# Performance work log

Measured on AMD Instinct MI355X. Metric: run time of the kernel, lower is better.

The kernel has to match this reference:

```python
import jax, jax.numpy as jnp
import numpy as np

N = 100000
E = 1600000
D = 128
H = 128


def gcn_conv(x, W, b, src, dst, n_nodes):
    # x: [N, Din] -> linear transform first (PyG GCNConv)
    h = x @ W  # [N, Dout]
    # add self loops
    loop = jnp.arange(n_nodes, dtype=src.dtype)
    s = jnp.concatenate([src, loop])
    d = jnp.concatenate([dst, loop])
    # symmetric normalization: deg computed on destination (col) with unit weights
    deg = jnp.zeros((n_nodes,), dtype=h.dtype).at[d].add(1.0)
    dinv = jnp.where(deg > 0, jax.lax.rsqrt(deg), 0.0)
    norm = dinv[s] * dinv[d]  # [E+N]
    msg = h[s] * norm[:, None]  # gather + scale
    out = jax.ops.segment_sum(msg, d, num_segments=n_nodes)
    return out + b


def setup_inputs() -> dict:
    key = jax.random.key(0)
    ks = jax.random.split(key, 8)
    x = jax.random.normal(ks[0], (N, D), dtype=jnp.float32)
    edge_index = jax.random.randint(ks[1], (2, E), 0, N, dtype=jnp.int32)
    sc = 1.0 / np.sqrt(D)
    gate_W = jax.random.uniform(ks[2], (D, D), jnp.float32, -sc, sc)
    gate_b = jax.random.uniform(ks[3], (D,), jnp.float32, -sc, sc)
    W1 = jax.random.normal(ks[4], (D, H), dtype=jnp.float32) * sc
    b1 = jnp.zeros((H,), jnp.float32)
    W2 = jax.random.normal(ks[5], (H, H), dtype=jnp.float32) * (1.0 / np.sqrt(H))
    b2 = jnp.zeros((H,), jnp.float32)
    return {"x": x, "edge_index": edge_index, "gate_W": gate_W, "gate_b": gate_b,
            "W1": W1, "b1": b1, "W2": W2, "b2": b2}


def reference(x, edge_index, gate_W, gate_b, W1, b1, W2, b2):
    src, dst = edge_index[0], edge_index[1]
    gate = jax.nn.sigmoid(x @ gate_W + gate_b)
    h = x * gate
    h = gcn_conv(h, W1, b1, src, dst, N)
    h = jax.nn.relu(h)
    h = gcn_conv(h, W2, b2, src, dst, N)
    return h
```

## Files before the change

### kernel.cpp

```cpp
#include <hip/hip_runtime.h>
#include <hip/hip_bf16.h>
#include <math.h>


#define BUCKET_SHIFT 8
#define BUCKET_W 256
#define CAP 4864
#define NB_MAX 512
#define OSTRIDE 136

typedef __attribute__((ext_vector_type(8))) short bf16x8;
typedef __attribute__((ext_vector_type(4))) float f32x4;

__device__ __forceinline__ unsigned short f2bf(float x) {
    unsigned int u = __float_as_uint(x);
    unsigned int r = (u + 0x7FFFu + ((u >> 16) & 1u)) >> 16;
    return (unsigned short)r;
}
__device__ __forceinline__ float blo(unsigned int u) { return __uint_as_float(u << 16); }
__device__ __forceinline__ float bhi(unsigned int u) { return __uint_as_float(u & 0xFFFF0000u); }

__device__ __forceinline__ void cvt_hilo8(const float* v, bf16x8& hi, bf16x8& lo) {
#pragma unroll
    for (int j = 0; j < 8; j++) {
        unsigned short h = f2bf(v[j]);
        float hf = __uint_as_float((unsigned int)h << 16);
        hi[j] = (short)h;
        lo[j] = (short)f2bf(v[j] - hf);
    }
}

__device__ __forceinline__ f32x4 MF(bf16x8 a, bf16x8 b, f32x4 c) {
    return __builtin_amdgcn_mfma_f32_16x16x32_bf16(a, b, c, 0, 0, 0);
}

__global__ __launch_bounds__(512)
void prepinit_kernel(const float* __restrict__ W0, const float* __restrict__ W1,
                     const float* __restrict__ W2, uint4* __restrict__ img,
                     int* __restrict__ bcursor, int NB) {
    int b = blockIdx.x, t = threadIdx.x;
    if (b < 12) {
        int idx = b * 512 + t;
        int c = idx & 127, kb = (idx >> 7) & 15, w = idx >> 11;
        const float* W = (w == 0) ? W0 : (w == 1) ? W1 : W2;
        bf16x8 hb;
#pragma unroll
        for (int j = 0; j < 8; j++) hb[j] = (short)f2bf(W[(size_t)(kb * 8 + j) * 128 + c]);
        img[w * 2048 + c * 16 + (kb ^ (c & 15))] = *(uint4*)&hb;
    } else {
        if (t < NB) bcursor[t] = 0;
    }
}

__device__ __forceinline__ void partition_body(char* smem, int b, int t,
                                               const int* __restrict__ src,
                                               const int* __restrict__ dst,
                                               int* __restrict__ bucketCursor,
                                               unsigned int* __restrict__ part,
                                               int E, int NB, int chunk) {
    int* hist  = (int*)smem;
    int* basec = hist + NB_MAX;
    int e0 = b * chunk;
    int e1 = min(E, e0 + chunk);

    for (int i = t; i < NB; i += 512) hist[i] = 0;
    __syncthreads();
    for (int e = e0 + t; e < e1; e += 512) {
        int bb = dst[e] >> BUCKET_SHIFT;
        atomicAdd(&hist[bb], 1);
    }
    __syncthreads();
    for (int i = t; i < NB; i += 512) {
        int c = hist[i];
        basec[i] = c ? atomicAdd(&bucketCursor[i], c) : 0;
    }
    __syncthreads();
    for (int i = t; i < NB; i += 512) hist[i] = 0;
    __syncthreads();
    for (int e = e0 + t; e < e1; e += 512) {
        int d = dst[e], s = src[e];
        int bb = d >> BUCKET_SHIFT;
        int r = atomicAdd(&hist[bb], 1);
        int pos = basec[bb] + r;
        if (pos < CAP)
            part[(size_t)bb * CAP + pos] = ((unsigned int)(d & (BUCKET_W - 1)) << 17) | (unsigned int)s;
    }
}

__device__ __forceinline__ void gate_body(char* smem, int gb, int t,
                                          const float* __restrict__ x,
                                          const uint4* __restrict__ gimg,
                                          const float* __restrict__ gate_b,
                                          unsigned short* __restrict__ hpack, int n) {
    uint4* Wl = (uint4*)smem;
    unsigned short* OutS = (unsigned short*)(smem + 32768);
    int lane = t & 63, wv = t >> 6;
    int blockRow = gb * 128;

    for (int idx = t; idx < 2048; idx += 512) Wl[idx] = gimg[idx];

    bf16x8 Ahi[4], Alo[4];
    {
        int arow = blockRow + wv * 16 + (lane & 15);
        const float* ap = x + (size_t)min(arow, n - 1) * 128 + (lane >> 4) * 8;
#pragma unroll
        for (int s = 0; s < 4; s++) {
            float v[8];
            *(float4*)&v[0] = *(const float4*)&ap[s * 32];
            *(float4*)&v[4] = *(const float4*)&ap[s * 32 + 4];
            cvt_hilo8(v, Ahi[s], Alo[s]);
        }
    }
    __syncthreads();

    f32x4 acc[8];
#pragma unroll
    for (int nt = 0; nt < 8; nt++) acc[nt] = (f32x4)(0.f);
#pragma unroll
    for (int s = 0; s < 4; s++) {
        int kb = s * 4 + (lane >> 4);
#pragma unroll
        for (int nt = 0; nt < 8; nt++) {
            int c = nt * 16 + (lane & 15);
            bf16x8 bh = *(bf16x8*)&Wl[c * 16 + (kb ^ (lane & 15))];
            acc[nt] = MF(Ahi[s], bh, acc[nt]);
            acc[nt] = MF(Alo[s], bh, acc[nt]);
        }
    }

    int rl0 = wv * 16 + (lane >> 4) * 4;
#pragma unroll
    for (int nt = 0; nt < 8; nt++) {
        int c = nt * 16 + (lane & 15);
        float gb2 = gate_b[c];
#pragma unroll
        for (int r = 0; r < 4; r++) {
            int grow = min(blockRow + rl0 + r, n - 1);
            float xv = x[(size_t)grow * 128 + c];
            float hv = xv / (1.f + __expf(-(acc[nt][r] + gb2)));
            OutS[(rl0 + r) * OSTRIDE + c] = f2bf(hv);
        }
    }
    __syncthreads();
    {
        int row = t >> 2;
        int c0 = (t & 3) * 32;
        int grow = blockRow + row;
        if (grow < n) {
#pragma unroll
            for (int j = 0; j < 4; j++) {
                uint4 v = *(uint4*)&OutS[row * OSTRIDE + c0 + j * 8];
                *(uint4*)&hpack[(size_t)grow * 128 + c0 + j * 8] = v;
            }
        }
    }
}

__global__ __launch_bounds__(512)
void pg_kernel(const int* __restrict__ src, const int* __restrict__ dst,
               int* __restrict__ bucketCursor, unsigned int* __restrict__ part,
               int E, int NB, int chunk,
               const float* __restrict__ x, const uint4* __restrict__ gimg,
               const float* __restrict__ gate_b, unsigned short* __restrict__ hpack, int n) {
    __shared__ __align__(16) char smem[67584];
    int b = blockIdx.x, t = threadIdx.x;
    if (b < 256) partition_body(smem, b, t, src, dst, bucketCursor, part, E, NB, chunk);
    else         gate_body(smem, b - 256, t, x, gimg, gate_b, hpack, n);
}

__global__ __launch_bounds__(512)
void bucket_scan_kernel(const int* __restrict__ bucketCursor,
                        int* __restrict__ bucketBase, int NB) {
    __shared__ int sm[NB_MAX];
    int t = threadIdx.x;
    int v = (t < NB) ? min(bucketCursor[t], CAP) : 0;
    sm[t] = v;
    __syncthreads();
    for (int off = 1; off < NB_MAX; off <<= 1) {
        int a = (t >= off) ? sm[t - off] : 0;
        __syncthreads();
        sm[t] += a;
        __syncthreads();
    }
    if (t < NB) bucketBase[t + 1] = sm[t];
    if (t == 0) bucketBase[0] = 0;
}

__device__ __forceinline__ void fill_body(char* smem, int b, int t,
                                          const unsigned int* __restrict__ part,
                                          const int* __restrict__ bucketBase,
                                          int* __restrict__ rowptr, float* __restrict__ dinv,
                                          int* __restrict__ col, int N, int NB) {
    unsigned int* eLDS = (unsigned int*)smem;
    int* deg  = (int*)(smem + CAP * 4);
    int* cur  = deg + BUCKET_W;
    int* wsum = cur + BUCKET_W;

    int base = bucketBase[b];
    int cnt = bucketBase[b + 1] - base;

    for (int i = t; i < cnt; i += 512) eLDS[i] = part[(size_t)b * CAP + i];
    if (t < 256) deg[t] = 0;
    __syncthreads();
    for (int i = t; i < cnt; i += 512) atomicAdd(&deg[eLDS[i] >> 17], 1);
    __syncthreads();

    int v = (t < 256) ? deg[t] : 0;
    int incl = v;
    int lane = t & 63, w = t >> 6;
    for (int off = 1; off < 64; off <<= 1) {
        int u = __shfl_up(incl, off, 64);
        if (lane >= off) incl += u;
    }
    if (lane == 63) wsum[w] = incl;
    __syncthreads();
    int add = 0;
#pragma unroll
    for (int j = 0; j < 4; j++) if (j < w) add += wsum[j];
    int excl = add + incl - v;
    if (t < 256) {
        cur[t] = excl;
        int gnode = b * BUCKET_W + t;
        if (gnode < N) {
            rowptr[gnode] = base + excl;
            dinv[gnode] = rsqrtf((float)(v + 1));
        }
    }
    if (b == NB - 1 && t == 0) rowptr[N] = base + cnt;
    __syncthreads();

    for (int i = t; i < cnt; i += 512) {
        unsigned int ev = eLDS[i];
        int dl = ev >> 17;
        int p = atomicAdd(&cur[dl], 1);
        col[base + p] = (int)(ev & 0x1FFFFu);
    }
}

__device__ __forceinline__ void gemm_body(char* smem, int gb, int t,
                                          const unsigned short* __restrict__ A,
                                          const uint4* __restrict__ wimg,
                                          unsigned short* __restrict__ g, int n) {
    uint4* Wl = (uint4*)smem;
    unsigned short* OutS = (unsigned short*)(smem + 32768);
    int lane = t & 63, wv = t >> 6;
    int blockRow = gb * 128;

    for (int idx = t; idx < 2048; idx += 512) Wl[idx] = wimg[idx];

    bf16x8 Af[4];
    {
        int arow = blockRow + wv * 16 + (lane & 15);
        const uint4* ap = (const uint4*)(A + (size_t)min(arow, n - 1) * 128);
#pragma unroll
        for (int s = 0; s < 4; s++) {
            uint4 u = ap[(lane >> 4) + s * 4];
            Af[s] = *(bf16x8*)&u;
        }
    }
    __syncthreads();

    f32x4 acc[8];
#pragma unroll
    for (int nt = 0; nt < 8; nt++) acc[nt] = (f32x4)(0.f);
#pragma unroll
    for (int s = 0; s < 4; s++) {
        int kb = s * 4 + (lane >> 4);
#pragma unroll
        for (int nt = 0; nt < 8; nt++) {
            int c = nt * 16 + (lane & 15);
            bf16x8 bh = *(bf16x8*)&Wl[c * 16 + (kb ^ (lane & 15))];
            acc[nt] = MF(Af[s], bh, acc[nt]);
        }
    }

    int rl0 = wv * 16 + (lane >> 4) * 4;
#pragma unroll
    for (int nt = 0; nt < 8; nt++) {
        int c = nt * 16 + (lane & 15);
#pragma unroll
        for (int r = 0; r < 4; r++)
            OutS[(rl0 + r) * OSTRIDE + c] = f2bf(acc[nt][r]);
    }
    __syncthreads();
    {
        int row = t >> 2;
        int c0 = (t & 3) * 32;
        int grow = blockRow + row;
        if (grow < n) {
#pragma unroll
            for (int j = 0; j < 4; j++) {
                uint4 v = *(uint4*)&OutS[row * OSTRIDE + c0 + j * 8];
                *(uint4*)&g[(size_t)grow * 128 + c0 + j * 8] = v;
            }
        }
    }
}

__global__ __launch_bounds__(512)
void fg_kernel(const unsigned int* __restrict__ part, const int* __restrict__ bucketBase,
               int* __restrict__ rowptr, float* __restrict__ dinv, int* __restrict__ col,
               int N, int NB,
               const unsigned short* __restrict__ A, const uint4* __restrict__ wimg,
               unsigned short* __restrict__ g) {
    __shared__ __align__(16) char smem[67584];
    int b = blockIdx.x, t = threadIdx.x;
    if (b < NB) fill_body(smem, b, t, part, bucketBase, rowptr, dinv, col, N, NB);
    else        gemm_body(smem, b - NB, t, A, wimg, g, N);
}

__global__ __launch_bounds__(256)
void spmm_gemm_kernel(const uint4* __restrict__ g16, const int* __restrict__ rowptr,
                      const int* __restrict__ col, const float* __restrict__ dinv,
                      const float* __restrict__ b1, const uint4* __restrict__ w2img,
                      unsigned short* __restrict__ g2, int n) {
    __shared__ __align__(16) char smem[16896];
    uint4* Hl = (uint4*)smem;
    unsigned short* OutS = (unsigned short*)(smem + 8192);

    int t = threadIdx.x;
    int blockRow = blockIdx.x * 32;

    int r = t >> 3, l = t & 7;
    int i = min(blockRow + r, n - 1);
    float di = dinv[i];

    float acc[16];
    {
        uint4 s0 = g16[(size_t)i * 16 + l];
        uint4 s1 = g16[(size_t)i * 16 + 8 + l];
        acc[0] = di * blo(s0.x);  acc[1] = di * bhi(s0.x);
        acc[2] = di * blo(s0.y);  acc[3] = di * bhi(s0.y);
        acc[4] = di * blo(s0.z);  acc[5] = di * bhi(s0.z);
        acc[6] = di * blo(s0.w);  acc[7] = di * bhi(s0.w);
        acc[8] = di * blo(s1.x);  acc[9] = di * bhi(s1.x);
        acc[10] = di * blo(s1.y); acc[11] = di * bhi(s1.y);
        acc[12] = di * blo(s1.z); acc[13] = di * bhi(s1.z);
        acc[14] = di * blo(s1.w); acc[15] = di * bhi(s1.w);
    }
    int e0 = rowptr[i], e1 = rowptr[i + 1];
    int e = e0;
    for (; e + 4 <= e1; e += 4) {
        int s0 = col[e], s1 = col[e + 1], s2 = col[e + 2], s3 = col[e + 3];
        uint4 a0 = g16[(size_t)s0 * 16 + l];
        uint4 a1 = g16[(size_t)s0 * 16 + 8 + l];
        uint4 c0 = g16[(size_t)s1 * 16 + l];
        uint4 c1 = g16[(size_t)s1 * 16 + 8 + l];
        uint4 d0 = g16[(size_t)s2 * 16 + l];
        uint4 d1 = g16[(size_t)s2 * 16 + 8 + l];
        uint4 f0 = g16[(size_t)s3 * 16 + l];
        uint4 f1 = g16[(size_t)s3 * 16 + 8 + l];
        float w0 = dinv[s0], w1 = dinv[s1], w2 = dinv[s2], w3 = dinv[s3];
        acc[0]  = fmaf(w0, blo(a0.x), fmaf(w1, blo(c0.x), fmaf(w2, blo(d0.x), fmaf(w3, blo(f0.x), acc[0]))));
        acc[1]  = fmaf(w0, bhi(a0.x), fmaf(w1, bhi(c0.x), fmaf(w2, bhi(d0.x), fmaf(w3, bhi(f0.x), acc[1]))));
        acc[2]  = fmaf(w0, blo(a0.y), fmaf(w1, blo(c0.y), fmaf(w2, blo(d0.y), fmaf(w3, blo(f0.y), acc[2]))));
        acc[3]  = fmaf(w0, bhi(a0.y), fmaf(w1, bhi(c0.y), fmaf(w2, bhi(d0.y), fmaf(w3, bhi(f0.y), acc[3]))));
        acc[4]  = fmaf(w0, blo(a0.z), fmaf(w1, blo(c0.z), fmaf(w2, blo(d0.z), fmaf(w3, blo(f0.z), acc[4]))));
        acc[5]  = fmaf(w0, bhi(a0.z), fmaf(w1, bhi(c0.z), fmaf(w2, bhi(d0.z), fmaf(w3, bhi(f0.z), acc[5]))));
        acc[6]  = fmaf(w0, blo(a0.w), fmaf(w1, blo(c0.w), fmaf(w2, blo(d0.w), fmaf(w3, blo(f0.w), acc[6]))));
        acc[7]  = fmaf(w0, bhi(a0.w), fmaf(w1, bhi(c0.w), fmaf(w2, bhi(d0.w), fmaf(w3, bhi(f0.w), acc[7]))));
        acc[8]  = fmaf(w0, blo(a1.x), fmaf(w1, blo(c1.x), fmaf(w2, blo(d1.x), fmaf(w3, blo(f1.x), acc[8]))));
        acc[9]  = fmaf(w0, bhi(a1.x), fmaf(w1, bhi(c1.x), fmaf(w2, bhi(d1.x), fmaf(w3, bhi(f1.x), acc[9]))));
        acc[10] = fmaf(w0, blo(a1.y), fmaf(w1, blo(c1.y), fmaf(w2, blo(d1.y), fmaf(w3, blo(f1.y), acc[10]))));
        acc[11] = fmaf(w0, bhi(a1.y), fmaf(w1, bhi(c1.y), fmaf(w2, bhi(d1.y), fmaf(w3, bhi(f1.y), acc[11]))));
        acc[12] = fmaf(w0, blo(a1.z), fmaf(w1, blo(c1.z), fmaf(w2, blo(d1.z), fmaf(w3, blo(f1.z), acc[12]))));
        acc[13] = fmaf(w0, bhi(a1.z), fmaf(w1, bhi(c1.z), fmaf(w2, bhi(d1.z), fmaf(w3, bhi(f1.z), acc[13]))));
        acc[14] = fmaf(w0, blo(a1.w), fmaf(w1, blo(c1.w), fmaf(w2, blo(d1.w), fmaf(w3, blo(f1.w), acc[14]))));
        acc[15] = fmaf(w0, bhi(a1.w), fmaf(w1, bhi(c1.w), fmaf(w2, bhi(d1.w), fmaf(w3, bhi(f1.w), acc[15]))));
    }
    for (; e < e1; e++) {
        int s0 = col[e];
        uint4 a0 = g16[(size_t)s0 * 16 + l];
        uint4 a1 = g16[(size_t)s0 * 16 + 8 + l];
        float w0 = dinv[s0];
        acc[0]  = fmaf(w0, blo(a0.x), acc[0]);  acc[1]  = fmaf(w0, bhi(a0.x), acc[1]);
        acc[2]  = fmaf(w0, blo(a0.y), acc[2]);  acc[3]  = fmaf(w0, bhi(a0.y), acc[3]);
        acc[4]  = fmaf(w0, blo(a0.z), acc[4]);  acc[5]  = fmaf(w0, bhi(a0.z), acc[5]);
        acc[6]  = fmaf(w0, blo(a0.w), acc[6]);  acc[7]  = fmaf(w0, bhi(a0.w), acc[7]);
        acc[8]  = fmaf(w0, blo(a1.x), acc[8]);  acc[9]  = fmaf(w0, bhi(a1.x), acc[9]);
        acc[10] = fmaf(w0, blo(a1.y), acc[10]); acc[11] = fmaf(w0, bhi(a1.y), acc[11]);
        acc[12] = fmaf(w0, blo(a1.z), acc[12]); acc[13] = fmaf(w0, bhi(a1.z), acc[13]);
        acc[14] = fmaf(w0, blo(a1.w), acc[14]); acc[15] = fmaf(w0, bhi(a1.w), acc[15]);
    }

    {
        const float* bp0 = b1 + l * 8;
        const float* bp1 = b1 + 64 + l * 8;
        float4 b00 = *(const float4*)&bp0[0], b01 = *(const float4*)&bp0[4];
        float4 b10 = *(const float4*)&bp1[0], b11 = *(const float4*)&bp1[4];
        float h[16];
        h[0] = fmaxf(fmaf(acc[0], di, b00.x), 0.f);
        h[1] = fmaxf(fmaf(acc[1], di, b00.y), 0.f);
        h[2] = fmaxf(fmaf(acc[2], di, b00.z), 0.f);
        h[3] = fmaxf(fmaf(acc[3], di, b00.w), 0.f);
        h[4] = fmaxf(fmaf(acc[4], di, b01.x), 0.f);
        h[5] = fmaxf(fmaf(acc[5], di, b01.y), 0.f);
        h[6] = fmaxf(fmaf(acc[6], di, b01.z), 0.f);
        h[7] = fmaxf(fmaf(acc[7], di, b01.w), 0.f);
        h[8] = fmaxf(fmaf(acc[8], di, b10.x), 0.f);
        h[9] = fmaxf(fmaf(acc[9], di, b10.y), 0.f);
        h[10] = fmaxf(fmaf(acc[10], di, b10.z), 0.f);
        h[11] = fmaxf(fmaf(acc[11], di, b10.w), 0.f);
        h[12] = fmaxf(fmaf(acc[12], di, b11.x), 0.f);
        h[13] = fmaxf(fmaf(acc[13], di, b11.y), 0.f);
        h[14] = fmaxf(fmaf(acc[14], di, b11.z), 0.f);
        h[15] = fmaxf(fmaf(acc[15], di, b11.w), 0.f);
        uint4 p0, p1;
        p0.x = (unsigned int)f2bf(h[0]) | ((unsigned int)f2bf(h[1]) << 16);
        p0.y = (unsigned int)f2bf(h[2]) | ((unsigned int)f2bf(h[3]) << 16);
        p0.z = (unsigned int)f2bf(h[4]) | ((unsigned int)f2bf(h[5]) << 16);
        p0.w = (unsigned int)f2bf(h[6]) | ((unsigned int)f2bf(h[7]) << 16);
        p1.x = (unsigned int)f2bf(h[8]) | ((unsigned int)f2bf(h[9]) << 16);
        p1.y = (unsigned int)f2bf(h[10]) | ((unsigned int)f2bf(h[11]) << 16);
        p1.z = (unsigned int)f2bf(h[12]) | ((unsigned int)f2bf(h[13]) << 16);
        p1.w = (unsigned int)f2bf(h[14]) | ((unsigned int)f2bf(h[15]) << 16);
        int sw = r & 15;
        Hl[r * 16 + (l ^ sw)] = p0;
        Hl[r * 16 + ((l + 8) ^ sw)] = p1;
    }
    __syncthreads();

    int lane = t & 63, wv = t >> 6;
    int rt = wv & 1, ch = wv >> 1;
    bf16x8 Af[4];
    {
        int arow = rt * 16 + (lane & 15);
        int asw = arow & 15;
#pragma unroll
        for (int s = 0; s < 4; s++) {
            int kb = s * 4 + (lane >> 4);
            uint4 u = Hl[arow * 16 + (kb ^ asw)];
            Af[s] = *(bf16x8*)&u;
        }
    }
    f32x4 acc2[4];
#pragma unroll
    for (int ntl = 0; ntl < 4; ntl++) acc2[ntl] = (f32x4)(0.f);
#pragma unroll
    for (int s = 0; s < 4; s++) {
        int kb = s * 4 + (lane >> 4);
#pragma unroll
        for (int ntl = 0; ntl < 4; ntl++) {
            int c = (ch * 4 + ntl) * 16 + (lane & 15);
            uint4 u = w2img[c * 16 + (kb ^ (lane & 15))];
            acc2[ntl] = MF(Af[s], *(bf16x8*)&u, acc2[ntl]);
        }
    }

    int rl0 = rt * 16 + (lane >> 4) * 4;
    float dr[4];
#pragma unroll
    for (int rr = 0; rr < 4; rr++) dr[rr] = dinv[min(blockRow + rl0 + rr, n - 1)];
#pragma unroll
    for (int ntl = 0; ntl < 4; ntl++) {
        int c = (ch * 4 + ntl) * 16 + (lane & 15);
#pragma unroll
        for (int rr = 0; rr < 4; rr++)
            OutS[(rl0 + rr) * OSTRIDE + c] = f2bf(acc2[ntl][rr] * dr[rr]);
    }
    __syncthreads();
    {
        int grow = blockRow + r;
        if (grow < n) {
            uint4 v0 = *(uint4*)&OutS[r * OSTRIDE + l * 16];
            uint4 v1 = *(uint4*)&OutS[r * OSTRIDE + l * 16 + 8];
            *(uint4*)&g2[(size_t)grow * 128 + l * 16] = v0;
            *(uint4*)&g2[(size_t)grow * 128 + l * 16 + 8] = v1;
        }
    }
}

__global__ void spmm_kernel(const uint4* __restrict__ g16, const int* __restrict__ rowptr,
                            const int* __restrict__ col, const float* __restrict__ dinv,
                            const float* __restrict__ bias, float* __restrict__ outv,
                            int n, int nhb) {
    int half = (blockIdx.x >= nhb) ? 1 : 0;
    int rb = blockIdx.x - half * nhb;
    int i = rb * 32 + (threadIdx.x >> 3);
    if (i >= n) return;
    int c = threadIdx.x & 7;

    const uint4* gp = g16 + half * 8 + c;
    float acc[8];
    uint4 sv = gp[(size_t)i * 16];
    acc[0] = blo(sv.x); acc[1] = bhi(sv.x);
    acc[2] = blo(sv.y); acc[3] = bhi(sv.y);
    acc[4] = blo(sv.z); acc[5] = bhi(sv.z);
    acc[6] = blo(sv.w); acc[7] = bhi(sv.w);

    int e0 = rowptr[i], e1 = rowptr[i + 1];
    int e = e0;
    for (; e + 8 <= e1; e += 8) {
        uint4 v0 = gp[(size_t)col[e] * 16];
        uint4 v1 = gp[(size_t)col[e + 1] * 16];
        uint4 v2 = gp[(size_t)col[e + 2] * 16];
        uint4 v3 = gp[(size_t)col[e + 3] * 16];
        uint4 v4 = gp[(size_t)col[e + 4] * 16];
        uint4 v5 = gp[(size_t)col[e + 5] * 16];
        uint4 v6 = gp[(size_t)col[e + 6] * 16];
        uint4 v7 = gp[(size_t)col[e + 7] * 16];
        acc[0] += ((blo(v0.x) + blo(v1.x)) + (blo(v2.x) + blo(v3.x))) +
                  ((blo(v4.x) + blo(v5.x)) + (blo(v6.x) + blo(v7.x)));
        acc[1] += ((bhi(v0.x) + bhi(v1.x)) + (bhi(v2.x) + bhi(v3.x))) +
                  ((bhi(v4.x) + bhi(v5.x)) + (bhi(v6.x) + bhi(v7.x)));
        acc[2] += ((blo(v0.y) + blo(v1.y)) + (blo(v2.y) + blo(v3.y))) +
                  ((blo(v4.y) + blo(v5.y)) + (blo(v6.y) + blo(v7.y)));
        acc[3] += ((bhi(v0.y) + bhi(v1.y)) + (bhi(v2.y) + bhi(v3.y))) +
                  ((bhi(v4.y) + bhi(v5.y)) + (bhi(v6.y) + bhi(v7.y)));
        acc[4] += ((blo(v0.z) + blo(v1.z)) + (blo(v2.z) + blo(v3.z))) +
                  ((blo(v4.z) + blo(v5.z)) + (blo(v6.z) + blo(v7.z)));
        acc[5] += ((bhi(v0.z) + bhi(v1.z)) + (bhi(v2.z) + bhi(v3.z))) +
                  ((bhi(v4.z) + bhi(v5.z)) + (bhi(v6.z) + bhi(v7.z)));
        acc[6] += ((blo(v0.w) + blo(v1.w)) + (blo(v2.w) + blo(v3.w))) +
                  ((blo(v4.w) + blo(v5.w)) + (blo(v6.w) + blo(v7.w)));
        acc[7] += ((bhi(v0.w) + bhi(v1.w)) + (bhi(v2.w) + bhi(v3.w))) +
                  ((bhi(v4.w) + bhi(v5.w)) + (bhi(v6.w) + bhi(v7.w)));
    }
    for (; e + 2 <= e1; e += 2) {
        uint4 v0 = gp[(size_t)col[e] * 16];
        uint4 v1 = gp[(size_t)col[e + 1] * 16];
        acc[0] += blo(v0.x) + blo(v1.x); acc[1] += bhi(v0.x) + bhi(v1.x);
        acc[2] += blo(v0.y) + blo(v1.y); acc[3] += bhi(v0.y) + bhi(v1.y);
        acc[4] += blo(v0.z) + blo(v1.z); acc[5] += bhi(v0.z) + bhi(v1.z);
        acc[6] += blo(v0.w) + blo(v1.w); acc[7] += bhi(v0.w) + bhi(v1.w);
    }
    if (e < e1) {
        uint4 v0 = gp[(size_t)col[e] * 16];
        acc[0] += blo(v0.x); acc[1] += bhi(v0.x);
        acc[2] += blo(v0.y); acc[3] += bhi(v0.y);
        acc[4] += blo(v0.z); acc[5] += bhi(v0.z);
        acc[6] += blo(v0.w); acc[7] += bhi(v0.w);
    }

    float di = dinv[i];
    const float4* b4 = (const float4*)(bias + half * 64);
    float4 bv0 = b4[c * 2], bv1 = b4[c * 2 + 1];
    float r0[8];
    r0[0] = fmaf(acc[0], di, bv0.x);
    r0[1] = fmaf(acc[1], di, bv0.y);
    r0[2] = fmaf(acc[2], di, bv0.z);
    r0[3] = fmaf(acc[3], di, bv0.w);
    r0[4] = fmaf(acc[4], di, bv1.x);
    r0[5] = fmaf(acc[5], di, bv1.y);
    r0[6] = fmaf(acc[6], di, bv1.z);
    r0[7] = fmaf(acc[7], di, bv1.w);
    float* o = outv + (size_t)i * 128 + half * 64 + c * 8;
    f32x4 a = *(f32x4*)&r0[0];
    f32x4 b = *(f32x4*)&r0[4];
    __builtin_nontemporal_store(a, (f32x4*)o);
    __builtin_nontemporal_store(b, (f32x4*)(o + 4));
}

extern "C" void kernel_launch(void* const* d_in, const int* in_sizes, int n_in,
                              void* d_out, int out_size, void* d_ws, size_t ws_size,
                              hipStream_t stream) {
    const float* x      = (const float*)d_in[0];
    const int*   ei     = (const int*)d_in[1];
    const float* gate_W = (const float*)d_in[2];
    const float* gate_b = (const float*)d_in[3];
    const float* W1     = (const float*)d_in[4];
    const float* b1     = (const float*)d_in[5];
    const float* W2     = (const float*)d_in[6];
    const float* b2     = (const float*)d_in[7];
    float* out = (float*)d_out;

    const int N = in_sizes[0] / 128;
    const int E = in_sizes[1] / 2;
    const int* src = ei;
    const int* dst = ei + E;
    const int NB = (N + BUCKET_W - 1) / BUCKET_W;

    char* p = (char*)d_ws;
    auto alloc = [&](size_t bytes) { char* q = p; p += (bytes + 255) & ~(size_t)255; return q; };
    int*   rowptr  = (int*)alloc(((size_t)N + 1) * 4);
    float* dinv    = (float*)alloc((size_t)N * 4);
    int*   colb    = (int*)alloc((size_t)E * 4);
    int*   bcursor = (int*)alloc((size_t)NB * 4);
    int*   bbase   = (int*)alloc(((size_t)NB + 1) * 4);
    uint4* wimg    = (uint4*)alloc((size_t)3 * 2048 * 16);
    unsigned int*   part   = (unsigned int*)alloc((size_t)NB * CAP * 4);
    unsigned short* hpack  = (unsigned short*)alloc((size_t)N * 128 * 2);
    unsigned short* g16    = (unsigned short*)alloc((size_t)N * 128 * 2);
    unsigned short* g2buf  = (unsigned short*)alloc((size_t)N * 128 * 2);

    const int pblocks = 256;
    const int chunk = (E + pblocks - 1) / pblocks;
    int gblocks = (N + 127) / 128;
    int fblocks = (N + 31) / 32;
    int nhb = (N + 31) / 32;

    prepinit_kernel<<<13, 512, 0, stream>>>(gate_W, W1, W2, wimg, bcursor, NB);
    pg_kernel<<<256 + gblocks, 512, 0, stream>>>(src, dst, bcursor, part, E, NB, chunk,
                                                 x, wimg, gate_b, hpack, N);
    bucket_scan_kernel<<<1, 512, 0, stream>>>(bcursor, bbase, NB);
    fg_kernel<<<NB + gblocks, 512, 0, stream>>>(part, bbase, rowptr, dinv, colb, N, NB,
                                                hpack, wimg + 2048, g16);
    spmm_gemm_kernel<<<fblocks, 256, 0, stream>>>((const uint4*)g16, rowptr, colb,
                                                  dinv, b1, wimg + 4096, g2buf, N);
    spmm_kernel<<<2 * nhb, 256, 0, stream>>>((const uint4*)g2buf, rowptr, colb,
                                             dinv, b2, out, N, nhb);
}
```

Measured before the change: 209.2 us.

## Pre-scale GEMM output by source dinv to drop per-edge dinv gathers

Degree counting and dinv computation move into the bucket scan kernel, which now launches one extra block per bucket. Because dinv is then ready before fg_kernel, the first-layer GEMM can multiply each output row by its node's dinv. This lets the first SpMM sum neighbor rows directly, without a random per-edge dinv[s] load and FMA. The cost is a second read of the partition buffer in the scan kernel, plus extra bf16 rounding after the scale is applied.

```diff
diff --git a/kernel.cpp b/kernel.cpp
--- a/kernel.cpp
+++ b/kernel.cpp
@@ -169,27 +169,43 @@
 }
 
 __global__ __launch_bounds__(512)
-void bucket_scan_kernel(const int* __restrict__ bucketCursor,
-                        int* __restrict__ bucketBase, int NB) {
+void scan_deg_kernel(const unsigned int* __restrict__ part,
+                     const int* __restrict__ bucketCursor,
+                     int* __restrict__ bucketBase, float* __restrict__ dinv,
+                     int NB, int N) {
     __shared__ int sm[NB_MAX];
-    int t = threadIdx.x;
-    int v = (t < NB) ? min(bucketCursor[t], CAP) : 0;
-    sm[t] = v;
-    __syncthreads();
-    for (int off = 1; off < NB_MAX; off <<= 1) {
-        int a = (t >= off) ? sm[t - off] : 0;
+    int b = blockIdx.x, t = threadIdx.x;
+    if (b < NB) {
+        int* deg = sm;
+        if (t < 256) deg[t] = 0;
         __syncthreads();
-        sm[t] += a;
+        int cnt = min(bucketCursor[b], CAP);
+        for (int i = t; i < cnt; i += 512)
+            atomicAdd(&deg[part[(size_t)b * CAP + i] >> 17], 1);
         __syncthreads();
-    }
-    if (t < NB) bucketBase[t + 1] = sm[t];
-    if (t == 0) bucketBase[0] = 0;
+        if (t < 256) {
+            int gnode = b * BUCKET_W + t;
+            if (gnode < N) dinv[gnode] = rsqrtf((float)(deg[t] + 1));
+        }
+    } else {
+        int v = (t < NB) ? min(bucketCursor[t], CAP) : 0;
+        sm[t] = v;
+        __syncthreads();
+        for (int off = 1; off < NB_MAX; off <<= 1) {
+            int a = (t >= off) ? sm[t - off] : 0;
+            __syncthreads();
+            sm[t] += a;
+            __syncthreads();
+        }
+        if (t < NB) bucketBase[t + 1] = sm[t];
+        if (t == 0) bucketBase[0] = 0;
+    }
 }
 
 __device__ __forceinline__ void fill_body(char* smem, int b, int t,
                                           const unsigned int* __restrict__ part,
                                           const int* __restrict__ bucketBase,
-                                          int* __restrict__ rowptr, float* __restrict__ dinv,
+                                          int* __restrict__ rowptr,
                                           int* __restrict__ col, int N, int NB) {
     unsigned int* eLDS = (unsigned int*)smem;
     int* deg  = (int*)(smem + CAP * 4);
@@ -221,10 +237,7 @@
     if (t < 256) {
         cur[t] = excl;
         int gnode = b * BUCKET_W + t;
-        if (gnode < N) {
-            rowptr[gnode] = base + excl;
-            dinv[gnode] = rsqrtf((float)(v + 1));
-        }
+        if (gnode < N) rowptr[gnode] = base + excl;
     }
     if (b == NB - 1 && t == 0) rowptr[N] = base + cnt;
     __syncthreads();
@@ -240,6 +253,7 @@
 __device__ __forceinline__ void gemm_body(char* smem, int gb, int t,
                                           const unsigned short* __restrict__ A,
                                           const uint4* __restrict__ wimg,
+                                          const float* __restrict__ dinv,
                                           unsigned short* __restrict__ g, int n) {
     uint4* Wl = (uint4*)smem;
     unsigned short* OutS = (unsigned short*)(smem + 32768);
@@ -275,12 +289,15 @@
     }
 
     int rl0 = wv * 16 + (lane >> 4) * 4;
+    float di[4];
+#pragma unroll
+    for (int r = 0; r < 4; r++) di[r] = dinv[min(blockRow + rl0 + r, n - 1)];
 #pragma unroll
     for (int nt = 0; nt < 8; nt++) {
         int c = nt * 16 + (lane & 15);
 #pragma unroll
         for (int r = 0; r < 4; r++)
-            OutS[(rl0 + r) * OSTRIDE + c] = f2bf(acc[nt][r]);
+            OutS[(rl0 + r) * OSTRIDE + c] = f2bf(acc[nt][r] * di[r]);
     }
     __syncthreads();
     {
@@ -299,14 +316,14 @@
 
 __global__ __launch_bounds__(512)
 void fg_kernel(const unsigned int* __restrict__ part, const int* __restrict__ bucketBase,
-               int* __restrict__ rowptr, float* __restrict__ dinv, int* __restrict__ col,
-               int N, int NB,
+               int* __restrict__ rowptr, const float* __restrict__ dinv,
+               int* __restrict__ col, int N, int NB,
                const unsigned short* __restrict__ A, const uint4* __restrict__ wimg,
                unsigned short* __restrict__ g) {
     __shared__ __align__(16) char smem[67584];
     int b = blockIdx.x, t = threadIdx.x;
-    if (b < NB) fill_body(smem, b, t, part, bucketBase, rowptr, dinv, col, N, NB);
-    else        gemm_body(smem, b - NB, t, A, wimg, g, N);
+    if (b < NB) fill_body(smem, b, t, part, bucketBase, rowptr, col, N, NB);
+    else        gemm_body(smem, b - NB, t, A, wimg, dinv, g, N);
 }
 
 __global__ __launch_bounds__(256)
@@ -329,14 +346,14 @@
     {
         uint4 s0 = g16[(size_t)i * 16 + l];
         uint4 s1 = g16[(size_t)i * 16 + 8 + l];
-        acc[0] = di * blo(s0.x);  acc[1] = di * bhi(s0.x);
-        acc[2] = di * blo(s0.y);  acc[3] = di * bhi(s0.y);
-        acc[4] = di * blo(s0.z);  acc[5] = di * bhi(s0.z);
-        acc[6] = di * blo(s0.w);  acc[7] = di * bhi(s0.w);
-        acc[8] = di * blo(s1.x);  acc[9] = di * bhi(s1.x);
-        acc[10] = di * blo(s1.y); acc[11] = di * bhi(s1.y);
-        acc[12] = di * blo(s1.z); acc[13] = di * bhi(s1.z);
-        acc[14] = di * blo(s1.w); acc[15] = di * bhi(s1.w);
+        acc[0] = blo(s0.x);  acc[1] = bhi(s0.x);
+        acc[2] = blo(s0.y);  acc[3] = bhi(s0.y);
+        acc[4] = blo(s0.z);  acc[5] = bhi(s0.z);
+        acc[6] = blo(s0.w);  acc[7] = bhi(s0.w);
+        acc[8] = blo(s1.x);  acc[9] = bhi(s1.x);
+        acc[10] = blo(s1.y); acc[11] = bhi(s1.y);
+        acc[12] = blo(s1.z); acc[13] = bhi(s1.z);
+        acc[14] = blo(s1.w); acc[15] = bhi(s1.w);
     }
     int e0 = rowptr[i], e1 = rowptr[i + 1];
     int e = e0;
@@ -350,37 +367,35 @@
         uint4 d1 = g16[(size_t)s2 * 16 + 8 + l];
         uint4 f0 = g16[(size_t)s3 * 16 + l];
         uint4 f1 = g16[(size_t)s3 * 16 + 8 + l];
-        float w0 = dinv[s0], w1 = dinv[s1], w2 = dinv[s2], w3 = dinv[s3];
-        acc[0]  = fmaf(w0, blo(a0.x), fmaf(w1, blo(c0.x), fmaf(w2, blo(d0.x), fmaf(w3, blo(f0.x), acc[0]))));
-        acc[1]  = fmaf(w0, bhi(a0.x), fmaf(w1, bhi(c0.x), fmaf(w2, bhi(d0.x), fmaf(w3, bhi(f0.x), acc[1]))));
-        acc[2]  = fmaf(w0, blo(a0.y), fmaf(w1, blo(c0.y), fmaf(w2, blo(d0.y), fmaf(w3, blo(f0.y), acc[2]))));
-        acc[3]  = fmaf(w0, bhi(a0.y), fmaf(w1, bhi(c0.y), fmaf(w2, bhi(d0.y), fmaf(w3, bhi(f0.y), acc[3]))));
-        acc[4]  = fmaf(w0, blo(a0.z), fmaf(w1, blo(c0.z), fmaf(w2, blo(d0.z), fmaf(w3, blo(f0.z), acc[4]))));
-        acc[5]  = fmaf(w0, bhi(a0.z), fmaf(w1, bhi(c0.z), fmaf(w2, bhi(d0.z), fmaf(w3, bhi(f0.z), acc[5]))));
-        acc[6]  = fmaf(w0, blo(a0.w), fmaf(w1, blo(c0.w), fmaf(w2, blo(d0.w), fmaf(w3, blo(f0.w), acc[6]))));
-        acc[7]  = fmaf(w0, bhi(a0.w), fmaf(w1, bhi(c0.w), fmaf(w2, bhi(d0.w), fmaf(w3, bhi(f0.w), acc[7]))));
-        acc[8]  = fmaf(w0, blo(a1.x), fmaf(w1, blo(c1.x), fmaf(w2, blo(d1.x), fmaf(w3, blo(f1.x), acc[8]))));
-        acc[9]  = fmaf(w0, bhi(a1.x), fmaf(w1, bhi(c1.x), fmaf(w2, bhi(d1.x), fmaf(w3, bhi(f1.x), acc[9]))));
-        acc[10] = fmaf(w0, blo(a1.y), fmaf(w1, blo(c1.y), fmaf(w2, blo(d1.y), fmaf(w3, blo(f1.y), acc[10]))));
-        acc[11] = fmaf(w0, bhi(a1.y), fmaf(w1, bhi(c1.y), fmaf(w2, bhi(d1.y), fmaf(w3, bhi(f1.y), acc[11]))));
-        acc[12] = fmaf(w0, blo(a1.z), fmaf(w1, blo(c1.z), fmaf(w2, blo(d1.z), fmaf(w3, blo(f1.z), acc[12]))));
-        acc[13] = fmaf(w0, bhi(a1.z), fmaf(w1, bhi(c1.z), fmaf(w2, bhi(d1.z), fmaf(w3, bhi(f1.z), acc[13]))));
-        acc[14] = fmaf(w0, blo(a1.w), fmaf(w1, blo(c1.w), fmaf(w2, blo(d1.w), fmaf(w3, blo(f1.w), acc[14]))));
-        acc[15] = fmaf(w0, bhi(a1.w), fmaf(w1, bhi(c1.w), fmaf(w2, bhi(d1.w), fmaf(w3, bhi(f1.w), acc[15]))));
+        acc[0]  += (blo(a0.x) + blo(c0.x)) + (blo(d0.x) + blo(f0.x));
+        acc[1]  += (bhi(a0.x) + bhi(c0.x)) + (bhi(d0.x) + bhi(f0.x));
+        acc[2]  += (blo(a0.y) + blo(c0.y)) + (blo(d0.y) + blo(f0.y));
+        acc[3]  += (bhi(a0.y) + bhi(c0.y)) + (bhi(d0.y) + bhi(f0.y));
+        acc[4]  += (blo(a0.z) + blo(c0.z)) + (blo(d0.z) + blo(f0.z));
+        acc[5]  += (bhi(a0.z) + bhi(c0.z)) + (bhi(d0.z) + bhi(f0.z));
+        acc[6]  += (blo(a0.w) + blo(c0.w)) + (blo(d0.w) + blo(f0.w));
+        acc[7]  += (bhi(a0.w) + bhi(c0.w)) + (bhi(d0.w) + bhi(f0.w));
+        acc[8]  += (blo(a1.x) + blo(c1.x)) + (blo(d1.x) + blo(f1.x));
+        acc[9]  += (bhi(a1.x) + bhi(c1.x)) + (bhi(d1.x) + bhi(f1.x));
+        acc[10] += (blo(a1.y) + blo(c1.y)) + (blo(d1.y) + blo(f1.y));
+        acc[11] += (bhi(a1.y) + bhi(c1.y)) + (bhi(d1.y) + bhi(f1.y));
+        acc[12] += (blo(a1.z) + blo(c1.z)) + (blo(d1.z) + blo(f1.z));
+        acc[13] += (bhi(a1.z) + bhi(c1.z)) + (bhi(d1.z) + bhi(f1.z));
+        acc[14] += (blo(a1.w) + blo(c1.w)) + (blo(d1.w) + blo(f1.w));
+        acc[15] += (bhi(a1.w) + bhi(c1.w)) + (bhi(d1.w) + bhi(f1.w));
     }
     for (; e < e1; e++) {
         int s0 = col[e];
         uint4 a0 = g16[(size_t)s0 * 16 + l];
         uint4 a1 = g16[(size_t)s0 * 16 + 8 + l];
-        float w0 = dinv[s0];
-        acc[0]  = fmaf(w0, blo(a0.x), acc[0]);  acc[1]  = fmaf(w0, bhi(a0.x), acc[1]);
-        acc[2]  = fmaf(w0, blo(a0.y), acc[2]);  acc[3]  = fmaf(w0, bhi(a0.y), acc[3]);
-        acc[4]  = fmaf(w0, blo(a0.z), acc[4]);  acc[5]  = fmaf(w0, bhi(a0.z), acc[5]);
-        acc[6]  = fmaf(w0, blo(a0.w), acc[6]);  acc[7]  = fmaf(w0, bhi(a0.w), acc[7]);
-        acc[8]  = fmaf(w0, blo(a1.x), acc[8]);  acc[9]  = fmaf(w0, bhi(a1.x), acc[9]);
-        acc[10] = fmaf(w0, blo(a1.y), acc[10]); acc[11] = fmaf(w0, bhi(a1.y), acc[11]);
-        acc[12] = fmaf(w0, blo(a1.z), acc[12]); acc[13] = fmaf(w0, bhi(a1.z), acc[13]);
-        acc[14] = fmaf(w0, blo(a1.w), acc[14]); acc[15] = fmaf(w0, bhi(a1.w), acc[15]);
+        acc[0]  += blo(a0.x);  acc[1]  += bhi(a0.x);
+        acc[2]  += blo(a0.y);  acc[3]  += bhi(a0.y);
+        acc[4]  += blo(a0.z);  acc[5]  += bhi(a0.z);
+        acc[6]  += blo(a0.w);  acc[7]  += bhi(a0.w);
+        acc[8]  += blo(a1.x);  acc[9]  += bhi(a1.x);
+        acc[10] += blo(a1.y);  acc[11] += bhi(a1.y);
+        acc[12] += blo(a1.z);  acc[13] += bhi(a1.z);
+        acc[14] += blo(a1.w);  acc[15] += bhi(a1.w);
     }
 
     {
@@ -592,7 +607,7 @@
     prepinit_kernel<<<13, 512, 0, stream>>>(gate_W, W1, W2, wimg, bcursor, NB);
     pg_kernel<<<256 + gblocks, 512, 0, stream>>>(src, dst, bcursor, part, E, NB, chunk,
                                                  x, wimg, gate_b, hpack, N);
-    bucket_scan_kernel<<<1, 512, 0, stream>>>(bcursor, bbase, NB);
+    scan_deg_kernel<<<NB + 1, 512, 0, stream>>>(part, bcursor, bbase, dinv, NB, N);
     fg_kernel<<<NB + gblocks, 512, 0, stream>>>(part, bbase, rowptr, dinv, colb, N, NB,
                                                 hpack, wimg + 2048, g16);
     spmm_gemm_kernel<<<fblocks, 256, 0, stream>>>((const uint4*)g16, rowptr, colb,
```

Result: no change. 212.1 us (+1.3%).
